# Performance work log

Measured on AMD Instinct MI355X. Metric: run time of the kernel, lower is better.

## Reference

```python
import jax, jax.numpy as jnp
import numpy as np

TAU = 0.9
TOPK = 8
NUM_LAYERS = 3


def _layer_norm(x, g, b, eps=1e-5):
    mu = jnp.mean(x, axis=-1, keepdims=True)
    var = jnp.var(x, axis=-1, keepdims=True)
    return (x - mu) / jnp.sqrt(var + eps) * g + b


def _forward(x, edge_index, Wi, bi, wp, Wa, ba, ln1_g, ln1_b, ln2_g, ln2_b,
             W1, b1, W2, b2, Wc, bc, Wo, bo):
    N = x.shape[0]
    H = Wi.shape[1]
    # input projection + relu
    x = jax.nn.relu(x @ Wi + bi)
    src, dst = edge_index[0], edge_index[1]
    # ---- priority pi (computed under no_grad, dummy_alpha = 1, x_prev = 0) ----
    delta_x = jnp.sum(jnp.abs(x), axis=1)                      # [N]
    neigh = jax.ops.segment_sum(delta_x[src], dst, num_segments=N)
    pi = jax.lax.stop_gradient(jax.nn.sigmoid(x @ wp + neigh))  # [N]
    # ---- add self loops (selected subgraph == full graph) ----
    loops = jnp.arange(N, dtype=src.dtype)
    src_e = jnp.concatenate([src, loops])
    dst_e = jnp.concatenate([dst, loops])
    Et = src_e.shape[0]
    # ---- edge attention logits: att_mlp(cat[h_i, h_j, p_j]) computed as split matvec ----
    a_dst = x @ Wa[:H]          # contribution of h_i = x[dst]
    a_src = x @ Wa[H:2 * H]     # contribution of h_j = x[src]
    e = a_dst[dst_e] + a_src[src_e] + pi[src_e] * Wa[2 * H] + ba[0]
    e = jax.nn.leaky_relu(e, 0.2) / TAU
    e = jnp.clip(e, -5.0, 5.0)
    exp_e = jnp.exp(e)
    denom = jax.ops.segment_sum(exp_e, dst_e, num_segments=N)
    alpha = exp_e / (denom[dst_e] + 1e-16)
    # ---- per-destination top-k sparsification + renormalization (vectorized) ----
    order = jnp.lexsort((-alpha, dst_e))       # sort by dst, then alpha descending
    dst_s = dst_e[order]
    alpha_s = alpha[order]
    pos = jnp.arange(Et)
    is_new = jnp.concatenate([jnp.ones((1,), bool), dst_s[1:] != dst_s[:-1]])
    grp_start = jax.lax.cummax(jnp.where(is_new, pos, 0))
    rank = pos - grp_start                     # rank within each dst group
    keep = rank < TOPK
    ksum = jax.ops.segment_sum(jnp.where(keep, alpha_s, 0.0), dst_s, num_segments=N)
    alpha_new_s = jnp.where(keep, alpha_s / (ksum[dst_s] + 1e-16), 0.0)
    alpha = jnp.zeros((Et,), x.dtype).at[order].set(alpha_new_s)
    # ---- prenorm blocks with priority-weighted conv (dropout = identity, eval) ----
    h = x
    for l in range(NUM_LAYERS):
        hn = _layer_norm(h, ln1_g[l], ln1_b[l])
        xp = hn @ Wc[l] + bc[l]                               # conv linear
        msg = xp[src_e] * alpha[:, None]                      # [Et, H]
        agg = jax.ops.segment_sum(msg, dst_e, num_segments=N)  # scatter-add
        h = h + jax.nn.relu(agg)
        h2 = _layer_norm(h, ln2_g[l], ln2_b[l])
        h2 = jax.nn.gelu(h2 @ W1[l] + b1[l], approximate=False) @ W2[l] + b2[l]
        h = h + h2
    return h @ Wo + bo


def setup_inputs() -> dict:
    key = jax.random.key(0)
    ks = jax.random.split(key, 10)
    N, E, IN, H, OUT, L, F = 50000, 400000, 256, 256, 64, 3, 512
    def nrm(k, shape, scale):
        return jax.random.normal(k, shape, jnp.float32) * scale
    return {
        "x": nrm(ks[0], (N, IN), 1.0),
        "edge_index": jax.random.randint(ks[1], (2, E), 0, N, dtype=jnp.int32),
        "Wi": nrm(ks[2], (IN, H), IN ** -0.5), "bi": jnp.zeros((H,), jnp.float32),
        "wp": nrm(ks[3], (H,), H ** -0.5),
        "Wa": nrm(ks[4], (2 * H + 1,), (2 * H + 1) ** -0.5), "ba": jnp.zeros((1,), jnp.float32),
        "ln1_g": jnp.ones((L, H), jnp.float32), "ln1_b": jnp.zeros((L, H), jnp.float32),
        "ln2_g": jnp.ones((L, H), jnp.float32), "ln2_b": jnp.zeros((L, H), jnp.float32),
        "W1": nrm(ks[5], (L, H, F), H ** -0.5), "b1": jnp.zeros((L, F), jnp.float32),
        "W2": nrm(ks[6], (L, F, H), F ** -0.5), "b2": jnp.zeros((L, H), jnp.float32),
        "Wc": nrm(ks[7], (L, H, H), H ** -0.5), "bc": jnp.zeros((L, H), jnp.float32),
        "Wo": nrm(ks[8], (H, OUT), H ** -0.5), "bo": jnp.zeros((OUT,), jnp.float32),
    }


def reference(x, edge_index, Wi, bi, wp, Wa, ba, ln1_g, ln1_b, ln2_g, ln2_b,
              W1, b1, W2, b2, Wc, bc, Wo, bo):
    return _forward(x, edge_index, Wi, bi, wp, Wa, ba, ln1_g, ln1_b, ln2_g, ln2_b,
                    W1, b1, W2, b2, Wc, bc, Wo, bo)
```

## Files before the change

### kernel.cpp

```cpp
#include <hip/hip_runtime.h>
#include <math.h>

#define TAUF 0.9f

typedef unsigned int u32;
typedef unsigned short ushort;
typedef __attribute__((ext_vector_type(8))) short short8;
typedef __attribute__((ext_vector_type(8))) _Float16 half8;
typedef __attribute__((ext_vector_type(4))) _Float16 half4;
typedef __attribute__((ext_vector_type(4))) float f32x4;
typedef __attribute__((ext_vector_type(4))) unsigned short us4;

__device__ __forceinline__ float wave_sum(float v) {
#pragma unroll
  for (int off = 32; off > 0; off >>= 1) v += __shfl_down(v, off, 64);
  return __shfl(v, 0, 64);
}

__device__ __forceinline__ ushort f2bf(float f) {
  u32 u = __builtin_bit_cast(u32, f);
  u32 r = (u + 0x7FFFu + ((u >> 16) & 1u)) >> 16;
  return (ushort)r;
}
__device__ __forceinline__ float bf2f(ushort s) {
  u32 u = ((u32)s) << 16;
  return __builtin_bit_cast(float, u);
}

__device__ __forceinline__ float gelu_f(float x) {
  float z = x * 0.70710678118654752f;
  float az = fabsf(z);
  float t = 1.f / fmaf(0.3275911f, az, 1.f);
  float poly = t * fmaf(t, fmaf(t, fmaf(t, fmaf(t, 1.061405429f, -1.453152027f),
                                        1.421413741f), -0.284496736f), 0.254829592f);
  float erfa = fmaf(-poly, __expf(-az * az), 1.f);
  float s = (z < 0.f) ? -erfa : erfa;
  return 0.5f * x * (1.f + s);
}

__device__ __forceinline__ void gload16(const void* g, void* l) {
  __builtin_amdgcn_global_load_lds(
      (const __attribute__((address_space(1))) u32*)g,
      (__attribute__((address_space(3))) u32*)l, 16, 0, 0);
}

__launch_bounds__(256, 2)
__global__ void gemm_in_mfma(const _Float16* __restrict__ Ah, const _Float16* __restrict__ Al,
                             const _Float16* __restrict__ Bh, const _Float16* __restrict__ Bl,
                             const float* __restrict__ bias, const float* __restrict__ Wa,
                             const float* __restrict__ wp, const float* __restrict__ g1,
                             const float* __restrict__ b1g, float* __restrict__ C,
                             ushort* __restrict__ hn, float* __restrict__ delta,
                             float* __restrict__ adst, float* __restrict__ asrc,
                             float* __restrict__ xwp, int M) {
  __shared__ char lds[81920];
  char* As_h = lds;
  char* As_l = lds + 8192;
  char* Bs_h = lds + 16384;
  char* Bs_l = lds + 49152;
  const int tid = threadIdx.x;
  const int wave = tid >> 6, lane = tid & 63;
  const int bm = blockIdx.x * 64;
  const int srow = lane >> 3;
  const int scol = (((lane & 7) ^ srow) << 3);

  f32x4 accH[4][4], accC[4][4];
#pragma unroll
  for (int i = 0; i < 4; ++i)
#pragma unroll
    for (int j = 0; j < 4; ++j) {
      accH[i][j] = (f32x4){0.f, 0.f, 0.f, 0.f};
      accC[i][j] = (f32x4){0.f, 0.f, 0.f, 0.f};
    }

  for (int k0 = 0; k0 < 256; k0 += 64) {
#pragma unroll
    for (int r = 0; r < 2; ++r) {
      const int ch = r * 4 + wave;
      int ar = bm + ch * 8 + srow;
      ar = (ar < M) ? ar : (M - 1);
      gload16(Ah + (size_t)ar * 256 + k0 + scol, As_h + ch * 1024);
      gload16(Al + (size_t)ar * 256 + k0 + scol, As_l + ch * 1024);
    }
#pragma unroll
    for (int r = 0; r < 8; ++r) {
      const int ch = r * 4 + wave;
      const int br = ch * 8 + srow;
      gload16(Bh + (size_t)br * 256 + k0 + scol, Bs_h + ch * 1024);
      gload16(Bl + (size_t)br * 256 + k0 + scol, Bs_l + ch * 1024);
    }
    __syncthreads();
#pragma unroll
    for (int kk = 0; kk < 2; ++kk) {
      const int c = (kk * 32 + (lane >> 4) * 8) * 2;
      half8 ah[4], bh[4];
#pragma unroll
      for (int mi = 0; mi < 4; ++mi) {
        const int rr = mi * 16 + (lane & 15);
        ah[mi] = *(const half8*)(As_h + rr * 128 + (c ^ ((rr & 7) << 4)));
      }
#pragma unroll
      for (int ni = 0; ni < 4; ++ni) {
        const int rr = wave * 64 + ni * 16 + (lane & 15);
        bh[ni] = *(const half8*)(Bs_h + rr * 128 + (c ^ ((rr & 7) << 4)));
      }
#pragma unroll
      for (int mi = 0; mi < 4; ++mi)
#pragma unroll
        for (int ni = 0; ni < 4; ++ni)
          accH[mi][ni] = __builtin_amdgcn_mfma_f32_16x16x32_f16(ah[mi], bh[ni],
                                                                accH[mi][ni], 0, 0, 0);
      half8 al[4];
#pragma unroll
      for (int mi = 0; mi < 4; ++mi) {
        const int rr = mi * 16 + (lane & 15);
        al[mi] = *(const half8*)(As_l + rr * 128 + (c ^ ((rr & 7) << 4)));
      }
#pragma unroll
      for (int mi = 0; mi < 4; ++mi)
#pragma unroll
        for (int ni = 0; ni < 4; ++ni)
          accC[mi][ni] = __builtin_amdgcn_mfma_f32_16x16x32_f16(al[mi], bh[ni],
                                                                accC[mi][ni], 0, 0, 0);
      half8 bl[4];
#pragma unroll
      for (int ni = 0; ni < 4; ++ni) {
        const int rr = wave * 64 + ni * 16 + (lane & 15);
        bl[ni] = *(const half8*)(Bs_l + rr * 128 + (c ^ ((rr & 7) << 4)));
      }
#pragma unroll
      for (int mi = 0; mi < 4; ++mi)
#pragma unroll
        for (int ni = 0; ni < 4; ++ni)
          accC[mi][ni] = __builtin_amdgcn_mfma_f32_16x16x32_f16(ah[mi], bl[ni],
                                                                accC[mi][ni], 0, 0, 0);
    }
    __syncthreads();
  }

  float bb[4], wa0[4], wa1[4], wpv[4], gg[4], gb[4];
#pragma unroll
  for (int ni = 0; ni < 4; ++ni) {
    const int c = wave * 64 + ni * 16 + (lane & 15);
    bb[ni] = bias[c]; wa0[ni] = Wa[c]; wa1[ni] = Wa[256 + c];
    wpv[ni] = wp[c]; gg[ni] = g1[c]; gb[ni] = b1g[c];
  }
  float* red = (float*)lds;
  float* muA = (float*)(lds + 5120);
  float* isA = (float*)(lds + 5376);
  const float inv = 1.f / 2048.f;
#pragma unroll
  for (int mi = 0; mi < 4; ++mi) {
#pragma unroll
    for (int reg = 0; reg < 4; ++reg) {
      const int lrow = mi * 16 + (lane >> 4) * 4 + reg;
      const int row = bm + lrow;
      float v[4];
      float p0 = 0.f, p1 = 0.f, p2 = 0.f, p3 = 0.f, p4 = 0.f;
#pragma unroll
      for (int ni = 0; ni < 4; ++ni) {
        float t = accH[mi][ni][reg] + accC[mi][ni][reg] * inv + bb[ni];
        t = fmaxf(t, 0.f);
        v[ni] = t;
        p0 += t; p1 += t * wa0[ni]; p2 += t * wa1[ni]; p3 += t * wpv[ni];
        p4 += t * t;
      }
      if (row < M) {
#pragma unroll
        for (int ni = 0; ni < 4; ++ni)
          C[(size_t)row * 256 + wave * 64 + ni * 16 + (lane & 15)] = v[ni];
      }
#pragma unroll
      for (int ni = 0; ni < 4; ++ni) accH[mi][ni][reg] = v[ni];
#pragma unroll
      for (int off = 1; off < 16; off <<= 1) {
        p0 += __shfl_xor(p0, off, 64);
        p1 += __shfl_xor(p1, off, 64);
        p2 += __shfl_xor(p2, off, 64);
        p3 += __shfl_xor(p3, off, 64);
        p4 += __shfl_xor(p4, off, 64);
      }
      if ((lane & 15) == 0) {
        red[(0 * 4 + wave) * 64 + lrow] = p0;
        red[(1 * 4 + wave) * 64 + lrow] = p1;
        red[(2 * 4 + wave) * 64 + lrow] = p2;
        red[(3 * 4 + wave) * 64 + lrow] = p3;
        red[(4 * 4 + wave) * 64 + lrow] = p4;
      }
    }
  }
  __syncthreads();
  if (tid < 64) {
    float s0 = 0.f, s1 = 0.f, s2 = 0.f, s3 = 0.f, s4 = 0.f;
#pragma unroll
    for (int w = 0; w < 4; ++w) {
      s0 += red[(0 * 4 + w) * 64 + tid];
      s1 += red[(1 * 4 + w) * 64 + tid];
      s2 += red[(2 * 4 + w) * 64 + tid];
      s3 += red[(3 * 4 + w) * 64 + tid];
      s4 += red[(4 * 4 + w) * 64 + tid];
    }
    const int row = bm + tid;
    if (row < M) {
      delta[row] = s0; adst[row] = s1; asrc[row] = s2; xwp[row] = s3;
    }
    float mu = s0 * (1.f / 256.f);
    muA[tid] = mu;
    isA[tid] = rsqrtf(s4 * (1.f / 256.f) - mu * mu + 1e-5f);
  }
  __syncthreads();
#pragma unroll
  for (int mi = 0; mi < 4; ++mi) {
#pragma unroll
    for (int reg = 0; reg < 4; ++reg) {
      const int lrow = mi * 16 + (lane >> 4) * 4 + reg;
      const int row = bm + lrow;
      if (row >= M) continue;
      const float mu = muA[lrow], is = isA[lrow];
#pragma unroll
      for (int ni = 0; ni < 4; ++ni) {
        const int col = wave * 64 + ni * 16 + (lane & 15);
        hn[(size_t)row * 256 + col] = f2bf((accH[mi][ni][reg] - mu) * is * gg[ni] + gb[ni]);
      }
    }
  }
}

__global__ void xsplit_k(const float* __restrict__ X, _Float16* __restrict__ Xh,
                         _Float16* __restrict__ Xl, int total4) {
  int i = blockIdx.x * 256 + threadIdx.x;
  if (i >= total4) return;
  float4 x = reinterpret_cast<const float4*>(X)[i];
  half4 h, l;
  float xs[4] = {x.x, x.y, x.z, x.w};
#pragma unroll
  for (int j = 0; j < 4; ++j) {
    _Float16 hv = (_Float16)xs[j];
    h[j] = hv;
    l[j] = (_Float16)((xs[j] - (float)hv) * 2048.f);
  }
  reinterpret_cast<half4*>(Xh)[i] = h;
  reinterpret_cast<half4*>(Xl)[i] = l;
}

template <int EPI>
__launch_bounds__(256)
__global__ void gemm_mfma(const ushort* __restrict__ A, const ushort* __restrict__ Bt,
                          const float* __restrict__ bias, ushort* __restrict__ Cb,
                          int M, int N, int K) {
  __shared__ ushort As[128 * 64];
  __shared__ ushort Bs[128 * 64];
  const int tid = threadIdx.x;
  const int wave = tid >> 6, lane = tid & 63;
  const int bm = blockIdx.x * 128, bn = blockIdx.y * 128;
  const int wm = (wave >> 1) * 64, wn = (wave & 1) * 64;
  const int srow = lane >> 3;
  const int scol = (((lane & 7) ^ srow) << 3);

  f32x4 acc[4][4];
#pragma unroll
  for (int i = 0; i < 4; ++i)
#pragma unroll
    for (int j = 0; j < 4; ++j) acc[i][j] = (f32x4){0.f, 0.f, 0.f, 0.f};

  for (int k0 = 0; k0 < K; k0 += 64) {
#pragma unroll
    for (int r = 0; r < 4; ++r) {
      const int ch = r * 4 + wave;
      int ar = bm + ch * 8 + srow;
      ar = (ar < M) ? ar : (M - 1);
      gload16(A + (size_t)ar * K + k0 + scol, (char*)As + ch * 1024);
      const int br = bn + ch * 8 + srow;
      gload16(Bt + (size_t)br * K + k0 + scol, (char*)Bs + ch * 1024);
    }
    __syncthreads();
#pragma unroll
    for (int kk = 0; kk < 2; ++kk) {
      const int c = (kk * 32 + (lane >> 4) * 8) * 2;
      short8 a[4];
#pragma unroll
      for (int mi = 0; mi < 4; ++mi) {
        const int rr = wm + mi * 16 + (lane & 15);
        a[mi] = *(const short8*)((const char*)As + rr * 128 + (c ^ ((rr & 7) << 4)));
      }
#pragma unroll
      for (int ni = 0; ni < 4; ++ni) {
        const int rr = wn + ni * 16 + (lane & 15);
        short8 b = *(const short8*)((const char*)Bs + rr * 128 + (c ^ ((rr & 7) << 4)));
#pragma unroll
        for (int mi = 0; mi < 4; ++mi)
          acc[mi][ni] = __builtin_amdgcn_mfma_f32_16x16x32_bf16(a[mi], b,
                                                                acc[mi][ni], 0, 0, 0);
      }
    }
    __syncthreads();
  }

  float bb[4];
#pragma unroll
  for (int ni = 0; ni < 4; ++ni) bb[ni] = bias[bn + wn + ni * 16 + (lane & 15)];
#pragma unroll
  for (int mi = 0; mi < 4; ++mi) {
#pragma unroll
    for (int reg = 0; reg < 4; ++reg) {
      const int row = bm + wm + mi * 16 + (lane >> 4) * 4 + reg;
      if (row >= M) continue;
#pragma unroll
      for (int ni = 0; ni < 4; ++ni) {
        const int col = bn + wn + ni * 16 + (lane & 15);
        float v = acc[mi][ni][reg] + bb[ni];
        if (EPI == 2) v = gelu_f(v);
        Cb[(size_t)row * N + col] = f2bf(v);
      }
    }
  }
}

template <int LAST>
__launch_bounds__(512, 4)
__global__ void gemm_ffn2ln(const ushort* __restrict__ A, const ushort* __restrict__ Bt,
                            const float* __restrict__ bias, const float* __restrict__ g1,
                            const float* __restrict__ b1g, float* __restrict__ h,
                            ushort* __restrict__ hn, int M) {
  __shared__ ushort As[128 * 64];
  __shared__ ushort Bs[256 * 64];
  const int tid = threadIdx.x;
  const int wave = tid >> 6, lane = tid & 63;
  const int bm = blockIdx.x * 128;
  const int wm = (wave >> 2) * 64, wn = (wave & 3) * 64;
  const int srow = lane >> 3;
  const int scol = (((lane & 7) ^ srow) << 3);

  f32x4 acc[4][4];
#pragma unroll
  for (int i = 0; i < 4; ++i)
#pragma unroll
    for (int j = 0; j < 4; ++j) acc[i][j] = (f32x4){0.f, 0.f, 0.f, 0.f};

  for (int k0 = 0; k0 < 512; k0 += 64) {
#pragma unroll
    for (int r = 0; r < 2; ++r) {
      const int ch = r * 8 + wave;
      int ar = bm + ch * 8 + srow;
      ar = (ar < M) ? ar : (M - 1);
      gload16(A + (size_t)ar * 512 + k0 + scol, (char*)As + ch * 1024);
    }
#pragma unroll
    for (int r = 0; r < 4; ++r) {
      const int ch = r * 8 + wave;
      const int br = ch * 8 + srow;
      gload16(Bt + (size_t)br * 512 + k0 + scol, (char*)Bs + ch * 1024);
    }
    __syncthreads();
#pragma unroll
    for (int kk = 0; kk < 2; ++kk) {
      const int c = (kk * 32 + (lane >> 4) * 8) * 2;
      short8 a[4];
#pragma unroll
      for (int mi = 0; mi < 4; ++mi) {
        const int rr = wm + mi * 16 + (lane & 15);
        a[mi] = *(const short8*)((const char*)As + rr * 128 + (c ^ ((rr & 7) << 4)));
      }
#pragma unroll
      for (int ni = 0; ni < 4; ++ni) {
        const int rr = wn + ni * 16 + (lane & 15);
        short8 b = *(const short8*)((const char*)Bs + rr * 128 + (c ^ ((rr & 7) << 4)));
#pragma unroll
        for (int mi = 0; mi < 4; ++mi)
          acc[mi][ni] = __builtin_amdgcn_mfma_f32_16x16x32_bf16(a[mi], b,
                                                                acc[mi][ni], 0, 0, 0);
      }
    }
    __syncthreads();
  }

  float bb[4];
#pragma unroll
  for (int ni = 0; ni < 4; ++ni) bb[ni] = bias[wn + ni * 16 + (lane & 15)];

  float* redS = (float*)As;
  float* redQ = redS + 512;
  float* muA  = redQ + 512;
  float* isA  = muA + 128;

#pragma unroll
  for (int mi = 0; mi < 4; ++mi) {
#pragma unroll
    for (int reg = 0; reg < 4; ++reg) {
      const int lrow = wm + mi * 16 + (lane >> 4) * 4 + reg;
      const int row = bm + lrow;
      const bool ok = (row < M);
      float pS = 0.f, pQ = 0.f;
#pragma unroll
      for (int ni = 0; ni < 4; ++ni) {
        const int col = wn + ni * 16 + (lane & 15);
        float t = acc[mi][ni][reg] + bb[ni];
        if (ok) t += h[(size_t)row * 256 + col];
        acc[mi][ni][reg] = t;
        if (LAST) {
          if (ok) hn[(size_t)row * 256 + col] = f2bf(t);
        } else {
          if (ok) h[(size_t)row * 256 + col] = t;
          pS += t;
          pQ += t * t;
        }
      }
      if (!LAST) {
#pragma unroll
        for (int off = 1; off < 16; off <<= 1) {
          pS += __shfl_xor(pS, off, 64);
          pQ += __shfl_xor(pQ, off, 64);
        }
        if ((lane & 15) == 0) {
          redS[(wave & 3) * 128 + lrow] = pS;
          redQ[(wave & 3) * 128 + lrow] = pQ;
        }
      }
    }
  }
  if (LAST) return;
  __syncthreads();
  if (tid < 128) {
    float S = redS[tid] + redS[128 + tid] + redS[256 + tid] + redS[384 + tid];
    float Q = redQ[tid] + redQ[128 + tid] + redQ[256 + tid] + redQ[384 + tid];
    float mu = S * (1.f / 256.f);
    muA[tid] = mu;
    isA[tid] = rsqrtf(Q * (1.f / 256.f) - mu * mu + 1e-5f);
  }
  __syncthreads();
  float gg[4], gb[4];
#pragma unroll
  for (int ni = 0; ni < 4; ++ni) {
    gg[ni] = g1[wn + ni * 16 + (lane & 15)];
    gb[ni] = b1g[wn + ni * 16 + (lane & 15)];
  }
#pragma unroll
  for (int mi = 0; mi < 4; ++mi) {
#pragma unroll
    for (int reg = 0; reg < 4; ++reg) {
      const int lrow = wm + mi * 16 + (lane >> 4) * 4 + reg;
      const int row = bm + lrow;
      if (row >= M) continue;
      const float mu = muA[lrow], is = isA[lrow];
#pragma unroll
      for (int ni = 0; ni < 4; ++ni) {
        const int col = wn + ni * 16 + (lane & 15);
        hn[(size_t)row * 256 + col] = f2bf((acc[mi][ni][reg] - mu) * is * gg[ni] + gb[ni]);
      }
    }
  }
}

__launch_bounds__(256)
__global__ void gemm_out(const ushort* __restrict__ A, const ushort* __restrict__ Bt,
                         const float* __restrict__ bias, float* __restrict__ C, int M) {
  __shared__ ushort As[128 * 64];
  __shared__ ushort Bs[64 * 64];
  const int tid = threadIdx.x;
  const int wave = tid >> 6, lane = tid & 63;
  const int bm = blockIdx.x * 128;
  const int wm = wave * 32;
  const int srow = lane >> 3;
  const int scol = (((lane & 7) ^ srow) << 3);
  f32x4 acc[2][4];
#pragma unroll
  for (int i = 0; i < 2; ++i)
#pragma unroll
    for (int j = 0; j < 4; ++j) acc[i][j] = (f32x4){0.f, 0.f, 0.f, 0.f};

  for (int k0 = 0; k0 < 256; k0 += 64) {
#pragma unroll
    for (int r = 0; r < 4; ++r) {
      const int ch = r * 4 + wave;
      int ar = bm + ch * 8 + srow;
      ar = (ar < M) ? ar : (M - 1);
      gload16(A + (size_t)ar * 256 + k0 + scol, (char*)As + ch * 1024);
    }
#pragma unroll
    for (int r = 0; r < 2; ++r) {
      const int ch = r * 4 + wave;
      const int br = ch * 8 + srow;
      gload16(Bt + (size_t)br * 256 + k0 + scol, (char*)Bs + ch * 1024);
    }
    __syncthreads();
#pragma unroll
    for (int kk = 0; kk < 2; ++kk) {
      const int c = (kk * 32 + (lane >> 4) * 8) * 2;
      short8 a[2], b[4];
#pragma unroll
      for (int mi = 0; mi < 2; ++mi) {
        const int rr = wm + mi * 16 + (lane & 15);
        a[mi] = *(const short8*)((const char*)As + rr * 128 + (c ^ ((rr & 7) << 4)));
      }
#pragma unroll
      for (int ni = 0; ni < 4; ++ni) {
        const int rr = ni * 16 + (lane & 15);
        b[ni] = *(const short8*)((const char*)Bs + rr * 128 + (c ^ ((rr & 7) << 4)));
      }
#pragma unroll
      for (int mi = 0; mi < 2; ++mi)
#pragma unroll
        for (int ni = 0; ni < 4; ++ni)
          acc[mi][ni] = __builtin_amdgcn_mfma_f32_16x16x32_bf16(a[mi], b[ni],
                                                                acc[mi][ni], 0, 0, 0);
    }
    __syncthreads();
  }
  float bb[4];
#pragma unroll
  for (int ni = 0; ni < 4; ++ni) bb[ni] = bias[ni * 16 + (lane & 15)];
#pragma unroll
  for (int mi = 0; mi < 2; ++mi) {
#pragma unroll
    for (int reg = 0; reg < 4; ++reg) {
      const int row = bm + wm + mi * 16 + (lane >> 4) * 4 + reg;
      if (row >= M) continue;
#pragma unroll
      for (int ni = 0; ni < 4; ++ni) {
        const int col = ni * 16 + (lane & 15);
        C[(size_t)row * 64 + col] = acc[mi][ni][reg] + bb[ni];
      }
    }
  }
}

#define W_IN 65536
#define W_TOTAL (196608 + 393216 + 393216 + 16384)
__global__ void prep_k(const float* __restrict__ Wi, const float* __restrict__ Wc,
                       const float* __restrict__ W1, const float* __restrict__ W2,
                       const float* __restrict__ Wo, _Float16* __restrict__ WiTh,
                       _Float16* __restrict__ WiTl, ushort* __restrict__ WcT,
                       ushort* __restrict__ W1T, ushort* __restrict__ W2T,
                       ushort* __restrict__ WoT, float* __restrict__ zbase, int zn) {
  int i = blockIdx.x * 256 + threadIdx.x;
  if (i < W_IN) {
    int n = i >> 8, k = i & 255;
    float w = Wi[(size_t)k * 256 + n];
    _Float16 hv = (_Float16)w;
    WiTh[i] = hv;
    WiTl[i] = (_Float16)((w - (float)hv) * 2048.f);
  } else if ((i -= W_IN) < W_TOTAL) {
    int j = i;
    if (j < 196608) {
      int l = j / 65536, r = j % 65536, n = r >> 8, k = r & 255;
      WcT[j] = f2bf(Wc[(size_t)l * 65536 + k * 256 + n]);
    } else if ((j -= 196608) < 393216) {
      int l = j / 131072, r = j % 131072, n = r >> 8, k = r & 255;
      W1T[j] = f2bf(W1[(size_t)l * 131072 + k * 512 + n]);
    } else if ((j -= 393216) < 393216) {
      int l = j / 131072, r = j % 131072, n = r >> 9, k = r & 511;
      W2T[j] = f2bf(W2[(size_t)l * 131072 + k * 256 + n]);
    } else {
      j -= 393216;
      int n = j >> 8, k = j & 255;
      WoT[j] = f2bf(Wo[k * 64 + n]);
    }
  } else {
    int z = i - W_TOTAL;
    if (z < zn) zbase[z] = 0.f;
  }
}

__global__ void neigh_k(const int* __restrict__ src, const int* __restrict__ dst,
                        const float* __restrict__ delta, float* __restrict__ neigh, int E) {
  int e = blockIdx.x * 256 + threadIdx.x;
  if (e < E) atomicAdd(&neigh[dst[e]], delta[src[e]]);
}

__global__ void logits_k(const int* __restrict__ src, const int* __restrict__ dst,
                         const float* __restrict__ adst, const float* __restrict__ asrc,
                         const float* __restrict__ xwp, const float* __restrict__ neigh,
                         const float* __restrict__ Wa, const float* __restrict__ ba,
                         float* __restrict__ expe, float* __restrict__ denom,
                         int* __restrict__ cnt, int* __restrict__ slots,
                         int E, int Et, int N) {
  int e = blockIdx.x * 256 + threadIdx.x;
  if (e >= Et) return;
  int s, d;
  if (e < E) { s = src[e]; d = dst[e]; } else { s = e - E; d = s; }
  float pis = 1.f / (1.f + expf(-(xwp[s] + neigh[s])));
  float v = adst[d] + asrc[s] + pis * Wa[512] + ba[0];
  v = (v >= 0.f ? v : 0.2f * v) / TAUF;
  v = fminf(fmaxf(v, -5.f), 5.f);
  float ex = expf(v);
  expe[e] = ex;
  atomicAdd(&denom[d], ex);
  int p = atomicAdd(&cnt[d], 1);
  if (p < 64) slots[(size_t)p * N + d] = e;
}

__device__ __forceinline__ bool better(float a, int e, float a2, int e2) {
  return a > a2 || (a == a2 && e < e2);
}

__global__ void topk_k(const int* __restrict__ cnt, const int* __restrict__ slots,
                       const float* __restrict__ expe, const float* __restrict__ denom,
                       const int* __restrict__ src, int* __restrict__ kcnt,
                       int* __restrict__ ksrc, float* __restrict__ kw, int N, int E) {
  int d = blockIdx.x * 256 + threadIdx.x;
  if (d >= N) return;
  int deg = min(cnt[d], 64);
  float D = denom[d] + 1e-16f;
  float av[8]; int ai[8]; int kc = 0;
  for (int t = 0; t < deg; ++t) {
    int e = slots[(size_t)t * N + d];
    float a = expe[e] / D;
    if (kc < 8) {
      int p = kc++;
      while (p > 0 && better(a, e, av[p - 1], ai[p - 1])) {
        av[p] = av[p - 1]; ai[p] = ai[p - 1]; --p;
      }
      av[p] = a; ai[p] = e;
    } else if (better(a, e, av[7], ai[7])) {
      int p = 7;
      while (p > 0 && better(a, e, av[p - 1], ai[p - 1])) {
        av[p] = av[p - 1]; ai[p] = ai[p - 1]; --p;
      }
      av[p] = a; ai[p] = e;
    }
  }
  float ks = 0.f;
  for (int j = 0; j < kc; ++j) ks += av[j];
  kcnt[d] = kc;
  for (int j = 0; j < kc; ++j) {
    int e = ai[j];
    ksrc[(size_t)d * 8 + j] = (e < E) ? src[e] : (e - E);
    kw[(size_t)d * 8 + j] = av[j] / (ks + 1e-16f);
  }
}

__global__ void agg_ln_k(const ushort* __restrict__ xp, const int* __restrict__ kcnt,
                         const int* __restrict__ ksrc, const float* __restrict__ kw,
                         const float* __restrict__ g, const float* __restrict__ b,
                         float* __restrict__ h, ushort* __restrict__ hn, int N) {
  int d = blockIdx.x * 4 + (threadIdx.x >> 6);
  if (d >= N) return;
  int lane = threadIdx.x & 63;
  int kc = kcnt[d];
  float a0 = 0.f, a1 = 0.f, a2 = 0.f, a3 = 0.f;
  for (int j = 0; j < kc; ++j) {
    int s = ksrc[(size_t)d * 8 + j];
    float w = kw[(size_t)d * 8 + j];
    us4 xv = *reinterpret_cast<const us4*>(xp + (size_t)s * 256 + lane * 4);
    a0 += w * bf2f(xv.x);
    a1 += w * bf2f(xv.y);
    a2 += w * bf2f(xv.z);
    a3 += w * bf2f(xv.w);
  }
  float* hr = h + (size_t)d * 256 + lane * 4;
  float4 hv = *reinterpret_cast<const float4*>(hr);
  float v0 = hv.x + fmaxf(a0, 0.f);
  float v1 = hv.y + fmaxf(a1, 0.f);
  float v2 = hv.z + fmaxf(a2, 0.f);
  float v3 = hv.w + fmaxf(a3, 0.f);
  *reinterpret_cast<float4*>(hr) = make_float4(v0, v1, v2, v3);
  float s = wave_sum(v0 + v1 + v2 + v3);
  float mu = s * (1.f / 256.f);
  float q = (v0 - mu) * (v0 - mu) + (v1 - mu) * (v1 - mu) +
            (v2 - mu) * (v2 - mu) + (v3 - mu) * (v3 - mu);
  q = wave_sum(q);
  float is = rsqrtf(q * (1.f / 256.f) + 1e-5f);
  float4 gg = *reinterpret_cast<const float4*>(g + lane * 4);
  float4 bb = *reinterpret_cast<const float4*>(b + lane * 4);
  us4 out;
  out.x = f2bf((v0 - mu) * is * gg.x + bb.x);
  out.y = f2bf((v1 - mu) * is * gg.y + bb.y);
  out.z = f2bf((v2 - mu) * is * gg.z + bb.z);
  out.w = f2bf((v3 - mu) * is * gg.w + bb.w);
  *reinterpret_cast<us4*>(hn + (size_t)d * 256 + lane * 4) = out;
}

extern "C" void kernel_launch(void* const* d_in, const int* in_sizes, int n_in,
                              void* d_out, int out_size, void* d_ws, size_t ws_size,
                              hipStream_t stream) {
  const float* X   = (const float*)d_in[0];
  const int*   EI  = (const int*)d_in[1];
  const float* Wi  = (const float*)d_in[2];
  const float* bi  = (const float*)d_in[3];
  const float* wp  = (const float*)d_in[4];
  const float* Wa  = (const float*)d_in[5];
  const float* ba  = (const float*)d_in[6];
  const float* l1g = (const float*)d_in[7];
  const float* l1b = (const float*)d_in[8];
  const float* l2g = (const float*)d_in[9];
  const float* l2b = (const float*)d_in[10];
  const float* W1  = (const float*)d_in[11];
  const float* b1  = (const float*)d_in[12];
  const float* W2  = (const float*)d_in[13];
  const float* b2  = (const float*)d_in[14];
  const float* Wc  = (const float*)d_in[15];
  const float* bc  = (const float*)d_in[16];
  const float* Wo  = (const float*)d_in[17];
  const float* bo  = (const float*)d_in[18];

  const int N = in_sizes[0] / 256;
  const int E = in_sizes[1] / 2;
  const int Et = E + N;
  const int* srcp = EI;
  const int* dstp = EI + E;

  float* ws = (float*)d_ws;
  size_t off = 0;
  auto alloc = [&](size_t n) { float* p = ws + off; off += n; return p; };
  const size_t NH = (size_t)N * 256;
  float*  h    = alloc(NH);
  ushort* hn   = (ushort*)alloc(NH / 2);
  ushort* xp   = (ushort*)alloc(NH / 2);
  float*  ualias = alloc(NH);
  ushort* u    = (ushort*)ualias;
  _Float16* Xh = (_Float16*)ualias;
  _Float16* Xl = Xh + NH;
  _Float16* WiTh = (_Float16*)alloc(65536 / 2);
  _Float16* WiTl = (_Float16*)alloc(65536 / 2);
  ushort* WcT  = (ushort*)alloc(3 * 65536 / 2);
  ushort* W1T  = (ushort*)alloc(3 * 131072 / 2);
  ushort* W2T  = (ushort*)alloc(3 * 131072 / 2);
  ushort* WoT  = (ushort*)alloc(16384 / 2);
  float* delta = alloc(N);
  float* adst  = alloc(N);
  float* asrc  = alloc(N);
  float* xwp   = alloc(N);
  float* expe  = alloc(Et);
  float* neigh = alloc(N);
  float* denom = alloc(N);
  int*   cnt   = (int*)alloc(N);
  int*   slots = (int*)alloc((size_t)N * 64);
  int*   kcnt  = (int*)alloc(N);
  int*   ksrc  = (int*)alloc((size_t)N * 8);
  float* kw    = alloc((size_t)N * 8);

  prep_k<<<(W_IN + W_TOTAL + 3 * N + 255) / 256, 256, 0, stream>>>(
      Wi, Wc, W1, W2, Wo, WiTh, WiTl, WcT, W1T, W2T, WoT, neigh, 3 * N);
  xsplit_k<<<((int)(NH / 4) + 255) / 256, 256, 0, stream>>>(X, Xh, Xl, (int)(NH / 4));

  gemm_in_mfma<<<(N + 63) / 64, 256, 0, stream>>>(
      Xh, Xl, WiTh, WiTl, bi, Wa, wp, l1g, l1b, h, hn,
      delta, adst, asrc, xwp, N);
  neigh_k<<<(E + 255) / 256, 256, 0, stream>>>(srcp, dstp, delta, neigh, E);
  logits_k<<<(Et + 255) / 256, 256, 0, stream>>>(srcp, dstp, adst, asrc, xwp, neigh,
                                                 Wa, ba, expe, denom, cnt, slots,
                                                 E, Et, N);
  topk_k<<<(N + 255) / 256, 256, 0, stream>>>(cnt, slots, expe, denom, srcp,
                                              kcnt, ksrc, kw, N, E);

  const int GM = (N + 127) / 128;
  for (int l = 0; l < 3; ++l) {
    gemm_mfma<1><<<dim3(GM, 2), 256, 0, stream>>>(
        hn, WcT + (size_t)l * 65536, bc + l * 256, xp, N, 256, 256);
    agg_ln_k<<<(N + 3) / 4, 256, 0, stream>>>(xp, kcnt, ksrc, kw,
                                              l2g + l * 256, l2b + l * 256, h, hn, N);
    gemm_mfma<2><<<dim3(GM, 4), 256, 0, stream>>>(
        hn, W1T + (size_t)l * 131072, b1 + l * 512, u, N, 512, 256);
    if (l < 2)
      gemm_ffn2ln<0><<<GM, 512, 0, stream>>>(
          u, W2T + (size_t)l * 131072, b2 + l * 256,
          l1g + (l + 1) * 256, l1b + (l + 1) * 256, h, hn, N);
    else
      gemm_ffn2ln<1><<<GM, 512, 0, stream>>>(
          u, W2T + (size_t)l * 131072, b2 + l * 256,
          nullptr, nullptr, h, hn, N);
  }
  gemm_out<<<(N + 127) / 128, 256, 0, stream>>>(hn, WoT, bo, (float*)d_out, N);
}
```

Measured before the change: 676.8 us.

## Aggregate before conv GEMM and fuse residual+LayerNorm into its epilogue

Uses the linearity of the convolution to gather and weight the top-k neighbour rows of hn first. The conv GEMM then runs on the aggregated rows, and ReLU, the residual add and LayerNorm move into a full-row (128x256) GEMM epilogue. This replaces the separate gather+LN kernel. It relies on the top-k weights summing to one so the bias term commutes. The FFN1 GEMM is retiled to 512-thread 128x256 blocks, and topk now always writes 8 padded slots so the gather loop can be fully unrolled. The trade-offs are an extra bf16 rounding of the aggregated input and LN variance computed as E[x^2]-mu^2.

```diff
diff --git a/kernel.cpp b/kernel.cpp
--- a/kernel.cpp
+++ b/kernel.cpp
@@ -10,12 +10,6 @@
 typedef __attribute__((ext_vector_type(4))) _Float16 half4;
 typedef __attribute__((ext_vector_type(4))) float f32x4;
 typedef __attribute__((ext_vector_type(4))) unsigned short us4;
-
-__device__ __forceinline__ float wave_sum(float v) {
-#pragma unroll
-  for (int off = 32; off > 0; off >>= 1) v += __shfl_down(v, off, 64);
-  return __shfl(v, 0, 64);
-}
 
 __device__ __forceinline__ ushort f2bf(float f) {
   u32 u = __builtin_bit_cast(u32, f);
@@ -243,17 +237,43 @@
   reinterpret_cast<half4*>(Xl)[i] = l;
 }
 
-template <int EPI>
-__launch_bounds__(256)
-__global__ void gemm_mfma(const ushort* __restrict__ A, const ushort* __restrict__ Bt,
-                          const float* __restrict__ bias, ushort* __restrict__ Cb,
-                          int M, int N, int K) {
+__global__ void gather_k(const ushort* __restrict__ hn, const int* __restrict__ ksrc,
+                         const float* __restrict__ kw, ushort* __restrict__ hagg, int N) {
+  int d = blockIdx.x * 4 + (threadIdx.x >> 6);
+  if (d >= N) return;
+  int lane = threadIdx.x & 63;
+  us4 xv[8];
+  float w[8];
+#pragma unroll
+  for (int j = 0; j < 8; ++j) {
+    int s = ksrc[(size_t)d * 8 + j];
+    w[j] = kw[(size_t)d * 8 + j];
+    xv[j] = *reinterpret_cast<const us4*>(hn + (size_t)s * 256 + lane * 4);
+  }
+  float a0 = 0.f, a1 = 0.f, a2 = 0.f, a3 = 0.f;
+#pragma unroll
+  for (int j = 0; j < 8; ++j) {
+    a0 += w[j] * bf2f(xv[j].x);
+    a1 += w[j] * bf2f(xv[j].y);
+    a2 += w[j] * bf2f(xv[j].z);
+    a3 += w[j] * bf2f(xv[j].w);
+  }
+  us4 o;
+  o.x = f2bf(a0); o.y = f2bf(a1); o.z = f2bf(a2); o.w = f2bf(a3);
+  *reinterpret_cast<us4*>(hagg + (size_t)d * 256 + lane * 4) = o;
+}
+
+__launch_bounds__(512, 4)
+__global__ void gemm_conv_aggln(const ushort* __restrict__ A, const ushort* __restrict__ Bt,
+                                const float* __restrict__ bias, const float* __restrict__ g2,
+                                const float* __restrict__ b2g, float* __restrict__ h,
+                                ushort* __restrict__ hn, int M) {
   __shared__ ushort As[128 * 64];
-  __shared__ ushort Bs[128 * 64];
+  __shared__ ushort Bs[256 * 64];
   const int tid = threadIdx.x;
   const int wave = tid >> 6, lane = tid & 63;
-  const int bm = blockIdx.x * 128, bn = blockIdx.y * 128;
-  const int wm = (wave >> 1) * 64, wn = (wave & 1) * 64;
+  const int bm = blockIdx.x * 128;
+  const int wm = (wave >> 2) * 64, wn = (wave & 3) * 64;
   const int srow = lane >> 3;
   const int scol = (((lane & 7) ^ srow) << 3);
 
@@ -263,15 +283,19 @@
 #pragma unroll
     for (int j = 0; j < 4; ++j) acc[i][j] = (f32x4){0.f, 0.f, 0.f, 0.f};
 
-  for (int k0 = 0; k0 < K; k0 += 64) {
-#pragma unroll
-    for (int r = 0; r < 4; ++r) {
-      const int ch = r * 4 + wave;
+  for (int k0 = 0; k0 < 256; k0 += 64) {
+#pragma unroll
+    for (int r = 0; r < 2; ++r) {
+      const int ch = r * 8 + wave;
       int ar = bm + ch * 8 + srow;
       ar = (ar < M) ? ar : (M - 1);
-      gload16(A + (size_t)ar * K + k0 + scol, (char*)As + ch * 1024);
-      const int br = bn + ch * 8 + srow;
-      gload16(Bt + (size_t)br * K + k0 + scol, (char*)Bs + ch * 1024);
+      gload16(A + (size_t)ar * 256 + k0 + scol, (char*)As + ch * 1024);
+    }
+#pragma unroll
+    for (int r = 0; r < 4; ++r) {
+      const int ch = r * 8 + wave;
+      const int br = ch * 8 + srow;
+      gload16(Bt + (size_t)br * 256 + k0 + scol, (char*)Bs + ch * 1024);
     }
     __syncthreads();
 #pragma unroll
@@ -298,6 +322,134 @@
 
   float bb[4];
 #pragma unroll
+  for (int ni = 0; ni < 4; ++ni) bb[ni] = bias[wn + ni * 16 + (lane & 15)];
+
+  float* redS = (float*)As;
+  float* redQ = redS + 512;
+  float* muA  = redQ + 512;
+  float* isA  = muA + 128;
+
+#pragma unroll
+  for (int mi = 0; mi < 4; ++mi) {
+#pragma unroll
+    for (int reg = 0; reg < 4; ++reg) {
+      const int lrow = wm + mi * 16 + (lane >> 4) * 4 + reg;
+      const int row = bm + lrow;
+      const bool ok = (row < M);
+      float pS = 0.f, pQ = 0.f;
+#pragma unroll
+      for (int ni = 0; ni < 4; ++ni) {
+        const int col = wn + ni * 16 + (lane & 15);
+        float t = fmaxf(acc[mi][ni][reg] + bb[ni], 0.f);
+        if (ok) {
+          t += h[(size_t)row * 256 + col];
+          h[(size_t)row * 256 + col] = t;
+        }
+        acc[mi][ni][reg] = t;
+        pS += t;
+        pQ += t * t;
+      }
+#pragma unroll
+      for (int off = 1; off < 16; off <<= 1) {
+        pS += __shfl_xor(pS, off, 64);
+        pQ += __shfl_xor(pQ, off, 64);
+      }
+      if ((lane & 15) == 0) {
+        redS[(wave & 3) * 128 + lrow] = pS;
+        redQ[(wave & 3) * 128 + lrow] = pQ;
+      }
+    }
+  }
+  __syncthreads();
+  if (tid < 128) {
+    float S = redS[tid] + redS[128 + tid] + redS[256 + tid] + redS[384 + tid];
+    float Q = redQ[tid] + redQ[128 + tid] + redQ[256 + tid] + redQ[384 + tid];
+    float mu = S * (1.f / 256.f);
+    muA[tid] = mu;
+    isA[tid] = rsqrtf(Q * (1.f / 256.f) - mu * mu + 1e-5f);
+  }
+  __syncthreads();
+  float gg[4], gb[4];
+#pragma unroll
+  for (int ni = 0; ni < 4; ++ni) {
+    gg[ni] = g2[wn + ni * 16 + (lane & 15)];
+    gb[ni] = b2g[wn + ni * 16 + (lane & 15)];
+  }
+#pragma unroll
+  for (int mi = 0; mi < 4; ++mi) {
+#pragma unroll
+    for (int reg = 0; reg < 4; ++reg) {
+      const int lrow = wm + mi * 16 + (lane >> 4) * 4 + reg;
+      const int row = bm + lrow;
+      if (row >= M) continue;
+      const float mu = muA[lrow], is = isA[lrow];
+#pragma unroll
+      for (int ni = 0; ni < 4; ++ni) {
+        const int col = wn + ni * 16 + (lane & 15);
+        hn[(size_t)row * 256 + col] = f2bf((acc[mi][ni][reg] - mu) * is * gg[ni] + gb[ni]);
+      }
+    }
+  }
+}
+
+__launch_bounds__(512, 4)
+__global__ void gemm_ffn1(const ushort* __restrict__ A, const ushort* __restrict__ Bt,
+                          const float* __restrict__ bias, ushort* __restrict__ u, int M) {
+  __shared__ ushort As[128 * 64];
+  __shared__ ushort Bs[256 * 64];
+  const int tid = threadIdx.x;
+  const int wave = tid >> 6, lane = tid & 63;
+  const int bm = blockIdx.x * 128;
+  const int bn = blockIdx.y * 256;
+  const int wm = (wave >> 2) * 64, wn = (wave & 3) * 64;
+  const int srow = lane >> 3;
+  const int scol = (((lane & 7) ^ srow) << 3);
+
+  f32x4 acc[4][4];
+#pragma unroll
+  for (int i = 0; i < 4; ++i)
+#pragma unroll
+    for (int j = 0; j < 4; ++j) acc[i][j] = (f32x4){0.f, 0.f, 0.f, 0.f};
+
+  for (int k0 = 0; k0 < 256; k0 += 64) {
+#pragma unroll
+    for (int r = 0; r < 2; ++r) {
+      const int ch = r * 8 + wave;
+      int ar = bm + ch * 8 + srow;
+      ar = (ar < M) ? ar : (M - 1);
+      gload16(A + (size_t)ar * 256 + k0 + scol, (char*)As + ch * 1024);
+    }
+#pragma unroll
+    for (int r = 0; r < 4; ++r) {
+      const int ch = r * 8 + wave;
+      const int br = bn + ch * 8 + srow;
+      gload16(Bt + (size_t)br * 256 + k0 + scol, (char*)Bs + ch * 1024);
+    }
+    __syncthreads();
+#pragma unroll
+    for (int kk = 0; kk < 2; ++kk) {
+      const int c = (kk * 32 + (lane >> 4) * 8) * 2;
+      short8 a[4];
+#pragma unroll
+      for (int mi = 0; mi < 4; ++mi) {
+        const int rr = wm + mi * 16 + (lane & 15);
+        a[mi] = *(const short8*)((const char*)As + rr * 128 + (c ^ ((rr & 7) << 4)));
+      }
+#pragma unroll
+      for (int ni = 0; ni < 4; ++ni) {
+        const int rr = wn + ni * 16 + (lane & 15);
+        short8 b = *(const short8*)((const char*)Bs + rr * 128 + (c ^ ((rr & 7) << 4)));
+#pragma unroll
+        for (int mi = 0; mi < 4; ++mi)
+          acc[mi][ni] = __builtin_amdgcn_mfma_f32_16x16x32_bf16(a[mi], b,
+                                                                acc[mi][ni], 0, 0, 0);
+      }
+    }
+    __syncthreads();
+  }
+
+  float bb[4];
+#pragma unroll
   for (int ni = 0; ni < 4; ++ni) bb[ni] = bias[bn + wn + ni * 16 + (lane & 15)];
 #pragma unroll
   for (int mi = 0; mi < 4; ++mi) {
@@ -308,9 +460,7 @@
 #pragma unroll
       for (int ni = 0; ni < 4; ++ni) {
         const int col = bn + wn + ni * 16 + (lane & 15);
-        float v = acc[mi][ni][reg] + bb[ni];
-        if (EPI == 2) v = gelu_f(v);
-        Cb[(size_t)row * N + col] = f2bf(v);
+        u[(size_t)row * 512 + col] = f2bf(gelu_f(acc[mi][ni][reg] + bb[ni]));
       }
     }
   }
@@ -595,8 +745,8 @@
 
 __global__ void topk_k(const int* __restrict__ cnt, const int* __restrict__ slots,
                        const float* __restrict__ expe, const float* __restrict__ denom,
-                       const int* __restrict__ src, int* __restrict__ kcnt,
-                       int* __restrict__ ksrc, float* __restrict__ kw, int N, int E) {
+                       const int* __restrict__ src, int* __restrict__ ksrc,
+                       float* __restrict__ kw, int N, int E) {
   int d = blockIdx.x * 256 + threadIdx.x;
   if (d >= N) return;
   int deg = min(cnt[d], 64);
@@ -621,53 +771,18 @@
   }
   float ks = 0.f;
   for (int j = 0; j < kc; ++j) ks += av[j];
-  kcnt[d] = kc;
-  for (int j = 0; j < kc; ++j) {
-    int e = ai[j];
-    ksrc[(size_t)d * 8 + j] = (e < E) ? src[e] : (e - E);
-    kw[(size_t)d * 8 + j] = av[j] / (ks + 1e-16f);
-  }
-}
-
-__global__ void agg_ln_k(const ushort* __restrict__ xp, const int* __restrict__ kcnt,
-                         const int* __restrict__ ksrc, const float* __restrict__ kw,
-                         const float* __restrict__ g, const float* __restrict__ b,
-                         float* __restrict__ h, ushort* __restrict__ hn, int N) {
-  int d = blockIdx.x * 4 + (threadIdx.x >> 6);
-  if (d >= N) return;
-  int lane = threadIdx.x & 63;
-  int kc = kcnt[d];
-  float a0 = 0.f, a1 = 0.f, a2 = 0.f, a3 = 0.f;
-  for (int j = 0; j < kc; ++j) {
-    int s = ksrc[(size_t)d * 8 + j];
-    float w = kw[(size_t)d * 8 + j];
-    us4 xv = *reinterpret_cast<const us4*>(xp + (size_t)s * 256 + lane * 4);
-    a0 += w * bf2f(xv.x);
-    a1 += w * bf2f(xv.y);
-    a2 += w * bf2f(xv.z);
-    a3 += w * bf2f(xv.w);
-  }
-  float* hr = h + (size_t)d * 256 + lane * 4;
-  float4 hv = *reinterpret_cast<const float4*>(hr);
-  float v0 = hv.x + fmaxf(a0, 0.f);
-  float v1 = hv.y + fmaxf(a1, 0.f);
-  float v2 = hv.z + fmaxf(a2, 0.f);
-  float v3 = hv.w + fmaxf(a3, 0.f);
-  *reinterpret_cast<float4*>(hr) = make_float4(v0, v1, v2, v3);
-  float s = wave_sum(v0 + v1 + v2 + v3);
-  float mu = s * (1.f / 256.f);
-  float q = (v0 - mu) * (v0 - mu) + (v1 - mu) * (v1 - mu) +
-            (v2 - mu) * (v2 - mu) + (v3 - mu) * (v3 - mu);
-  q = wave_sum(q);
-  float is = rsqrtf(q * (1.f / 256.f) + 1e-5f);
-  float4 gg = *reinterpret_cast<const float4*>(g + lane * 4);
-  float4 bb = *reinterpret_cast<const float4*>(b + lane * 4);
-  us4 out;
-  out.x = f2bf((v0 - mu) * is * gg.x + bb.x);
-  out.y = f2bf((v1 - mu) * is * gg.y + bb.y);
-  out.z = f2bf((v2 - mu) * is * gg.z + bb.z);
-  out.w = f2bf((v3 - mu) * is * gg.w + bb.w);
-  *reinterpret_cast<us4*>(hn + (size_t)d * 256 + lane * 4) = out;
+  float inv = 1.f / (ks + 1e-16f);
+#pragma unroll
+  for (int j = 0; j < 8; ++j) {
+    if (j < kc) {
+      int e = ai[j];
+      ksrc[(size_t)d * 8 + j] = (e < E) ? src[e] : (e - E);
+      kw[(size_t)d * 8 + j] = av[j] * inv;
+    } else {
+      ksrc[(size_t)d * 8 + j] = 0;
+      kw[(size_t)d * 8 + j] = 0.f;
+    }
+  }
 }
 
 extern "C" void kernel_launch(void* const* d_in, const int* in_sizes, int n_in,
@@ -705,7 +820,7 @@
   const size_t NH = (size_t)N * 256;
   float*  h    = alloc(NH);
   ushort* hn   = (ushort*)alloc(NH / 2);
-  ushort* xp   = (ushort*)alloc(NH / 2);
+  ushort* hagg = (ushort*)alloc(NH / 2);
   float*  ualias = alloc(NH);
   ushort* u    = (ushort*)ualias;
   _Float16* Xh = (_Float16*)ualias;
@@ -725,7 +840,6 @@
   float* denom = alloc(N);
   int*   cnt   = (int*)alloc(N);
   int*   slots = (int*)alloc((size_t)N * 64);
-  int*   kcnt  = (int*)alloc(N);
   int*   ksrc  = (int*)alloc((size_t)N * 8);
   float* kw    = alloc((size_t)N * 8);
 
@@ -741,16 +855,16 @@
                                                  Wa, ba, expe, denom, cnt, slots,
                                                  E, Et, N);
   topk_k<<<(N + 255) / 256, 256, 0, stream>>>(cnt, slots, expe, denom, srcp,
-                                              kcnt, ksrc, kw, N, E);
+                                              ksrc, kw, N, E);
 
   const int GM = (N + 127) / 128;
   for (int l = 0; l < 3; ++l) {
-    gemm_mfma<1><<<dim3(GM, 2), 256, 0, stream>>>(
-        hn, WcT + (size_t)l * 65536, bc + l * 256, xp, N, 256, 256);
-    agg_ln_k<<<(N + 3) / 4, 256, 0, stream>>>(xp, kcnt, ksrc, kw,
-                                              l2g + l * 256, l2b + l * 256, h, hn, N);
-    gemm_mfma<2><<<dim3(GM, 4), 256, 0, stream>>>(
-        hn, W1T + (size_t)l * 131072, b1 + l * 512, u, N, 512, 256);
+    gather_k<<<(N + 3) / 4, 256, 0, stream>>>(hn, ksrc, kw, hagg, N);
+    gemm_conv_aggln<<<GM, 512, 0, stream>>>(
+        hagg, WcT + (size_t)l * 65536, bc + l * 256,
+        l2g + l * 256, l2b + l * 256, h, hn, N);
+    gemm_ffn1<<<dim3(GM, 2), 512, 0, stream>>>(
+        hn, W1T + (size_t)l * 131072, b1 + l * 512, u, N);
     if (l < 2)
       gemm_ffn2ln<0><<<GM, 512, 0, stream>>>(
           u, W2T + (size_t)l * 131072, b2 + l * 256,
```

New measurement: 646.3 us. -4.5%, faster.
